# Kernel optimization log

Hardware: AMD Instinct MI355X
Metric: run time of the kernel (lower is better)

Reference implementation:

```python
import jax, jax.numpy as jnp
import numpy as np

B, LQ, LK, D = 2, 2048, 2048, 1024
H, DK, DV = 16, 64, 64
EPS = 1e-6


def setup_inputs() -> dict:
    key = jax.random.key(0)
    ks = jax.random.split(key, 12)
    s = 1.0 / np.sqrt(D)
    return {
        "PE_states": jax.random.normal(ks[0], (B, LK, D), jnp.float32),
        "global_state": jax.random.normal(ks[1], (B, LQ, D), jnp.float32),
        "PE_statements": jax.random.normal(ks[2], (B, LK, D), jnp.float32),
        "PE_operators": jax.random.normal(ks[3], (B, LK, D), jnp.float32),
        "PE_solution_scores": jax.random.uniform(ks[4], (B, LK), jnp.float32),
        "mask": jax.random.randint(ks[5], (B, LQ, LK), 0, 2, jnp.int32),
        "w_q": jax.random.normal(ks[6], (D, H * DK), jnp.float32) * s,
        "w_k": jax.random.normal(ks[7], (D, H * DK), jnp.float32) * s,
        "w_v": jax.random.normal(ks[8], (D, H * DV), jnp.float32) * s,
        "w_fc": jax.random.normal(ks[9], (H * DV, D), jnp.float32) * s,
        "ln_gamma": jnp.ones((D,), jnp.float32),
        "ln_beta": jnp.zeros((D,), jnp.float32),
    }


def _layer_norm(x, gamma, beta):
    mu = jnp.mean(x, axis=-1, keepdims=True)
    var = jnp.mean(jnp.square(x - mu), axis=-1, keepdims=True)
    return (x - mu) * jax.lax.rsqrt(var + EPS) * gamma + beta


def reference(PE_states, global_state, PE_statements, PE_operators,
              PE_solution_scores, mask, w_q, w_k, w_v, w_fc, ln_gamma, ln_beta):
    # att_type == 'ca_sc', query_mode == 'PE', dropout == 0
    residual = global_state  # [B, LQ, D]
    q = (global_state @ w_q).reshape(B, LQ, H, DK).transpose(0, 2, 1, 3)   # bhqd
    k = (PE_states @ w_k).reshape(B, LK, H, DK).transpose(0, 2, 1, 3)      # bhkd
    v_s = (PE_statements @ w_v).reshape(B, LK, H, DV).transpose(0, 2, 1, 3)
    v_o = (PE_operators @ w_v).reshape(B, LK, H, DV).transpose(0, 2, 1, 3)

    temp = jnp.asarray(DK, jnp.float32) ** 0.5
    attn = jnp.einsum('bhqd,bhkd->bhqk', q / temp, k)  # [B,H,LQ,LK]
    # PE_solution_scores: per-key bias broadcast over heads and queries
    attn = (attn + PE_solution_scores[:, None, None, :]) / 2.0
    attn = jnp.where(mask[:, None, :, :] == 0, jnp.float32(-1e9), attn)
    attn = jax.nn.softmax(attn, axis=-1)

    def head_out(v):
        o = jnp.einsum('bhqk,bhkd->bhqd', attn, v)
        o = o.transpose(0, 2, 1, 3).reshape(B, LQ, H * DV)
        o = o @ w_fc + residual
        return _layer_norm(o, ln_gamma, ln_beta)

    statement_pred = head_out(v_s)
    operator_pred = head_out(v_o)
    return statement_pred, operator_pred
```

## Files before the change

kernel.cpp:

```cpp
#include <hip/hip_runtime.h>


typedef unsigned short u16;
typedef unsigned int   u32;
typedef unsigned long long u64;

typedef __attribute__((ext_vector_type(8))) short frag_ab;
typedef __attribute__((ext_vector_type(4))) float frag_cd;
typedef __attribute__((ext_vector_type(16))) float f32x16;
typedef __attribute__((ext_vector_type(8))) unsigned short u16x8;
typedef __attribute__((ext_vector_type(4))) unsigned short u16x4;
typedef __attribute__((ext_vector_type(2))) unsigned int u32x2;
typedef __attribute__((ext_vector_type(4))) int int4v;

__device__ __forceinline__ u16 f2bf(float f) {
    u32 x = __builtin_bit_cast(u32, f);
    return (u16)((x + 0x7fffu + ((x >> 16) & 1u)) >> 16);
}

__device__ __forceinline__ u32 pkbf(float a, float b) {
    return __builtin_amdgcn_perm(__builtin_bit_cast(u32, b),
                                 __builtin_bit_cast(u32, a), 0x07060302u);
}

#define GLDS16(gsrc, ldst)                                                     \
    __builtin_amdgcn_global_load_lds(                                          \
        (const __attribute__((address_space(1))) void*)(gsrc),                 \
        (__attribute__((address_space(3))) void*)(ldst), 16, 0, 0)

#define MFMA32(a, b, c) __builtin_amdgcn_mfma_f32_32x32x16_bf16(a, b, c, 0, 0, 0)

__global__ __launch_bounds__(256) void prep_kernel(
    const float* __restrict__ in0, const float* __restrict__ in1,
    const float* __restrict__ in2, const float* __restrict__ in3,
    u16* __restrict__ Ab4,
    const float* __restrict__ w_q, const float* __restrict__ w_k,
    const float* __restrict__ w_v, const float* __restrict__ w_fc,
    u16* __restrict__ wqT, u16* __restrict__ wkT,
    u16* __restrict__ wvT, u16* __restrict__ wfcT,
    const int* __restrict__ mask, u64* __restrict__ bits)
{
    __shared__ u16 tile[32][33];
    const int bid = blockIdx.x;
    const int tid = threadIdx.x;
    if (bid < 8192) {
        int z = bid >> 11;
        const float* in = z == 0 ? in0 : z == 1 ? in1 : z == 2 ? in2 : in3;
        u16* o = Ab4 + (size_t)z * 4194304;
        size_t i = ((size_t)(bid & 2047) * 256 + tid) * 8;
        float4 f0 = *(const float4*)(in + i);
        float4 f1 = *(const float4*)(in + i + 4);
        u16x8 t;
        t[0] = f2bf(f0.x); t[1] = f2bf(f0.y); t[2] = f2bf(f0.z); t[3] = f2bf(f0.w);
        t[4] = f2bf(f1.x); t[5] = f2bf(f1.y); t[6] = f2bf(f1.z); t[7] = f2bf(f1.w);
        *(u16x8*)(o + i) = t;
    } else if (bid < 12288) {
        int t = bid - 8192;
        int z = t >> 10;
        const float* in = z == 0 ? w_q : z == 1 ? w_k : z == 2 ? w_v : w_fc;
        u16* out = z == 0 ? wqT : z == 1 ? wkT : z == 2 ? wvT : wfcT;
        int bx = (t & 31) * 32, by = ((t >> 5) & 31) * 32;
        int tx = tid & 31, ty = tid >> 5;
        for (int i = 0; i < 32; i += 8)
            tile[ty + i][tx] = f2bf(in[(size_t)(by + ty + i) * 1024 + bx + tx]);
        __syncthreads();
        for (int i = 0; i < 32; i += 8)
            out[(size_t)(bx + ty + i) * 1024 + by + tx] = tile[tx][ty + i];
    } else {
        int pb = bid - 12288;
        int wv = tid >> 6, ln = tid & 63;
        long long base = (long long)pb * 2048 + wv * 512;
        for (int j = 0; j < 8; j++) {
            int v = mask[base + j * 64 + ln];
            u64 bl = __ballot(v != 0);
            if (ln == 0) bits[(base >> 6) + j] = bl;
        }
    }
}

__device__ __forceinline__ void gemm256_core(
    const u16* __restrict__ A, const u16* __restrict__ BT,
    int bm, int bn, u16* ring, frag_cd acc[8][4])
{
    const int tid = threadIdx.x;
    const int wave = tid >> 6, lane = tid & 63;
    const int ln15 = lane & 15, quad = lane >> 4;
    const int wr = wave >> 2, wc = wave & 3;

    auto stage = [&](int t) {
        u16* slot = ring + (t & 3) * 16384;
        size_t col = (size_t)t * 32 + quad * 8;
        for (int s = 0; s < 4; s++) {
            int f = wave * 4 + s;
            if (f < 16)
                GLDS16(&A[(size_t)(bm + f * 16 + ln15) * 1024 + col], slot + f * 512);
            else
                GLDS16(&BT[(size_t)(bn + (f - 16) * 16 + ln15) * 1024 + col],
                       slot + 8192 + (f - 16) * 512);
        }
    };

    stage(0); stage(1); stage(2);

    for (int t = 0; t < 32; t++) {
        if (t < 30)       asm volatile("s_waitcnt vmcnt(8) lgkmcnt(0)" ::: "memory");
        else if (t == 30) asm volatile("s_waitcnt vmcnt(4) lgkmcnt(0)" ::: "memory");
        else              asm volatile("s_waitcnt vmcnt(0) lgkmcnt(0)" ::: "memory");
        __builtin_amdgcn_s_barrier();
        __builtin_amdgcn_sched_barrier(0);
        if (t < 29) stage(t + 3);
        const u16* slot = ring + (t & 3) * 16384;
        const u16* aBase = slot + wr * 8 * 512;
        const u16* bBase = slot + 8192 + wc * 4 * 512;
        frag_ab b[4];
#pragma unroll
        for (int j = 0; j < 4; j++)
            b[j] = *(const frag_ab*)(bBase + j * 512 + lane * 8);
#pragma unroll
        for (int m = 0; m < 8; m++) {
            frag_ab a = *(const frag_ab*)(aBase + m * 512 + lane * 8);
            __builtin_amdgcn_s_setprio(1);
#pragma unroll
            for (int j = 0; j < 4; j++)
                acc[m][j] = __builtin_amdgcn_mfma_f32_16x16x32_bf16(a, b[j], acc[m][j], 0, 0, 0);
            __builtin_amdgcn_s_setprio(0);
        }
    }
}

__global__ __launch_bounds__(512, 2) void proj_gemm_kernel(
    const u16* __restrict__ Ab4,
    const u16* __restrict__ wqT, const u16* __restrict__ wkT, const u16* __restrict__ wvT,
    u16* __restrict__ Qb, u16* __restrict__ Kb,
    u16* __restrict__ VsT_g, u16* __restrict__ VoT_g)
{
    __shared__ alignas(16) u16 ring[4 * 16384];
    const int bid = blockIdx.x;
    const int xcd = bid & 7;
    const int w = bid >> 3;
    const int z = xcd >> 1;
    const int bm = ((xcd & 1) * 8 + (w >> 2)) * 256;
    const int bn = (w & 3) * 256;
    const u16* A = Ab4 + (size_t)z * 4194304;
    const u16* BT = z == 0 ? wqT : z == 1 ? wkT : wvT;
    frag_cd acc[8][4] = {};
    gemm256_core(A, BT, bm, bn, ring, acc);

    const int lane = threadIdx.x & 63;
    const int wave = threadIdx.x >> 6;
    const int ln15 = lane & 15, quad = lane >> 4;
    const int wr = wave >> 2, wc = wave & 3;
    if (z < 2) {
        u16* C = z == 0 ? Qb : Kb;
        const float qsc = z == 0 ? 0.09016844f : 1.0f;
        for (int m = 0; m < 8; m++) for (int j = 0; j < 4; j++) {
            int row0 = bm + wr * 128 + m * 16 + quad * 4;
            int col = bn + wc * 64 + j * 16 + ln15;
            for (int r = 0; r < 4; r++)
                C[(size_t)(row0 + r) * 1024 + col] = f2bf(acc[m][j][r] * qsc);
        }
    } else {
        u16* C = z == 2 ? VsT_g : VoT_g;
        for (int m = 0; m < 8; m++) for (int j = 0; j < 4; j++) {
            int row0 = bm + wr * 128 + m * 16 + quad * 4;
            int col = bn + wc * 64 + j * 16 + ln15;
            u16x4 t;
            for (int r = 0; r < 4; r++) t[r] = f2bf(acc[m][j][r]);
            *(u16x4*)&C[(size_t)col * 4096 + row0] = t;
        }
    }
}

__global__ __launch_bounds__(512, 2) void fc_gemm_kernel(
    const u16* __restrict__ Osb, const u16* __restrict__ wfcT,
    const float* __restrict__ resid, float* __restrict__ preLN)
{
    __shared__ alignas(16) u16 ring[4 * 12288];
    const int bm = blockIdx.x * 256, bn = blockIdx.y * 128;
    const int tid = threadIdx.x;
    const int wave = tid >> 6, lane = tid & 63;
    const int ln15 = lane & 15, quad = lane >> 4;
    const int wr = wave >> 2, wc = wave & 3;
    const u16* A = Osb;
    frag_cd acc[8][2] = {};

    auto stage = [&](int t) {
        u16* slot = ring + (t & 3) * 12288;
        size_t col = (size_t)t * 32 + quad * 8;
        for (int s = 0; s < 3; s++) {
            int f = wave * 3 + s;
            if (f < 16)
                GLDS16(&A[(size_t)(bm + f * 16 + ln15) * 1024 + col], slot + f * 512);
            else
                GLDS16(&wfcT[(size_t)(bn + (f - 16) * 16 + ln15) * 1024 + col],
                       slot + 8192 + (f - 16) * 512);
        }
    };

    stage(0); stage(1); stage(2);

    for (int t = 0; t < 32; t++) {
        if (t < 30)       asm volatile("s_waitcnt vmcnt(6) lgkmcnt(0)" ::: "memory");
        else if (t == 30) asm volatile("s_waitcnt vmcnt(3) lgkmcnt(0)" ::: "memory");
        else              asm volatile("s_waitcnt vmcnt(0) lgkmcnt(0)" ::: "memory");
        __builtin_amdgcn_s_barrier();
        __builtin_amdgcn_sched_barrier(0);
        if (t < 29) stage(t + 3);
        const u16* slot = ring + (t & 3) * 12288;
        const u16* aBase = slot + wr * 8 * 512;
        const u16* bBase = slot + 8192 + wc * 2 * 512;
        frag_ab b[2];
#pragma unroll
        for (int j = 0; j < 2; j++)
            b[j] = *(const frag_ab*)(bBase + j * 512 + lane * 8);
#pragma unroll
        for (int m = 0; m < 8; m++) {
            frag_ab a = *(const frag_ab*)(aBase + m * 512 + lane * 8);
            __builtin_amdgcn_s_setprio(1);
#pragma unroll
            for (int j = 0; j < 2; j++)
                acc[m][j] = __builtin_amdgcn_mfma_f32_16x16x32_bf16(a, b[j], acc[m][j], 0, 0, 0);
            __builtin_amdgcn_s_setprio(0);
        }
    }

    for (int m = 0; m < 8; m++) for (int j = 0; j < 2; j++) {
        int row0 = bm + wr * 128 + m * 16 + quad * 4;
        int col = bn + wc * 32 + j * 16 + ln15;
        for (int r = 0; r < 4; r++) {
            int row = row0 + r;
            preLN[(size_t)row * 1024 + col] =
                acc[m][j][r] + resid[(size_t)(row & 4095) * 1024 + col];
        }
    }
}

__device__ __forceinline__ void flash_stage(
    const u16* __restrict__ Kp, const u16* __restrict__ VsT, const u16* __restrict__ VoT,
    int b, int h, int kt, int wave, int ln31, int hi, u16* buf)
{
    const int k0 = kt * 64;
    for (int s = 0; s < 6; s++) {
        int t = wave * 6 + s;
        const u16* g;
        if (t < 8) {
            int n = t >> 2, ks = t & 3;
            g = &Kp[(size_t)(b * 2048 + k0 + n * 32 + ln31) * 1024 + h * 64 + ks * 16 + hi * 8];
        } else if (t < 16) {
            int dt = (t >> 2) & 1, sk = t & 3;
            g = &VsT[(size_t)(h * 64 + dt * 32 + ln31) * 4096 + b * 2048 + k0 + sk * 16 + hi * 8];
        } else {
            int dt = (t >> 2) & 1, sk = t & 3;
            g = &VoT[(size_t)(h * 64 + dt * 32 + ln31) * 4096 + b * 2048 + k0 + sk * 16 + hi * 8];
        }
        GLDS16(g, buf + t * 512);
    }
}

__global__ __launch_bounds__(256, 2) void flash_kernel(
    const u16* __restrict__ Q, const u16* __restrict__ Kp,
    const u16* __restrict__ VsT_g, const u16* __restrict__ VoT_g,
    const float* __restrict__ scores, const u64* __restrict__ mbits,
    u16* __restrict__ Os, u16* __restrict__ Oo)
{
    __shared__ alignas(16) u16 KV[2][24 * 512];
    const int bid = blockIdx.x;
    const int xcd = bid & 7;
    const int qt = (bid >> 3) & 15;
    const int g = xcd + 8 * (bid >> 7);
    const int h = g & 15, b = g >> 4;
    const int tid = threadIdx.x;
    const int wave = tid >> 6, lane = tid & 63;
    const int ln31 = lane & 31, hi = lane >> 5;
    const int qbase = b * 2048 + qt * 128 + wave * 32;
    const int qrow = qbase + ln31;

    frag_ab aq0, aq1, aq2, aq3;
    {
        const u16* qp = &Q[(size_t)qrow * 1024 + h * 64 + hi * 8];
        aq0 = *(const frag_ab*)(qp);
        aq1 = *(const frag_ab*)(qp + 16);
        aq2 = *(const frag_ab*)(qp + 32);
        aq3 = *(const frag_ab*)(qp + 48);
    }
    frag_ab bbias = {};
    bbias[0] = (short)0x3F80; bbias[1] = (short)0x3F80;

    f32x16 os0 = {}, os1 = {}, oo0 = {}, oo1 = {};
    float l0 = 0.f, l1 = 0.f;
    const int shl4 = 4 - 4 * hi;

    auto softmax16 = [&](f32x16& s, u32 wa, float& lacc) {
#pragma unroll
        for (int r = 0; r < 16; r++) {
            const int bitc = (r & 3) + 8 * (r >> 2);
            u32 m = (u32)(((int)(wa << (27 - bitc))) >> 31);
            float e = __builtin_amdgcn_exp2f(s[r]);
            u32 pb = __builtin_bit_cast(u32, e) & m;
            float pf = __builtin_bit_cast(float, pb);
            lacc += pf;
            s[r] = pf;
        }
    };

    flash_stage(Kp, VsT_g, VoT_g, b, h, 0, wave, ln31, hi, KV[0]);

    for (int kt = 0; kt < 32; kt++) {
        const int p = kt & 1;
        float sc0f = scores[b * 2048 + kt * 64 + ln31];
        float sc1f = scores[b * 2048 + kt * 64 + 32 + ln31];
        u64 w = mbits[(size_t)qrow * 32 + kt];
        __syncthreads();
        if (kt < 31)
            flash_stage(Kp, VsT_g, VoT_g, b, h, kt + 1, wave, ln31, hi, KV[p ^ 1]);
        const u16* bufp = KV[p];

        frag_ab ab0 = {}, ab1 = {};
        if (!hi) {
            float t0 = sc0f * 0.72134752f;
            u16 c0 = f2bf(t0);
            ab0[0] = (short)c0;
            ab0[1] = (short)f2bf(t0 - __builtin_bit_cast(float, (u32)c0 << 16));
            float t1 = sc1f * 0.72134752f;
            u16 c1 = f2bf(t1);
            ab1[0] = (short)c1;
            ab1[1] = (short)f2bf(t1 - __builtin_bit_cast(float, (u32)c1 << 16));
        }

        f32x16 sacc0 = {}, sacc1 = {};
        sacc0 = MFMA32(ab0, bbias, sacc0);
        sacc1 = MFMA32(ab1, bbias, sacc1);
#pragma unroll
        for (int ks = 0; ks < 4; ks++) {
            frag_ab ak0 = *(const frag_ab*)(bufp + (0 * 4 + ks) * 512 + lane * 8);
            frag_ab ak1 = *(const frag_ab*)(bufp + (1 * 4 + ks) * 512 + lane * 8);
            frag_ab q = ks == 0 ? aq0 : ks == 1 ? aq1 : ks == 2 ? aq2 : aq3;
            sacc0 = MFMA32(ak0, q, sacc0);
            sacc1 = MFMA32(ak1, q, sacc1);
        }

        u32 wa0 = ((u32)w) << shl4;
        u32 wa1 = ((u32)(w >> 32)) << shl4;
        softmax16(sacc0, wa0, l0);
        softmax16(sacc1, wa1, l1);

#pragma unroll
        for (int sk = 0; sk < 4; sk++) {
            const f32x16& ps = (sk < 2) ? sacc0 : sacc1;
            const int e0 = (sk & 1) * 8;
            u32 a0 = pkbf(ps[e0 + 0], ps[e0 + 1]);
            u32 a1 = pkbf(ps[e0 + 2], ps[e0 + 3]);
            u32 b0 = pkbf(ps[e0 + 4], ps[e0 + 5]);
            u32 b1 = pkbf(ps[e0 + 6], ps[e0 + 7]);
            u32x2 r0 = __builtin_amdgcn_permlane32_swap(a0, b0, false, false);
            u32x2 r1 = __builtin_amdgcn_permlane32_swap(a1, b1, false, false);
            int4v iv;
            iv[0] = (int)r0[0]; iv[1] = (int)r1[0];
            iv[2] = (int)r0[1]; iv[3] = (int)r1[1];
            frag_ab ap = __builtin_bit_cast(frag_ab, iv);
            frag_ab bs0 = *(const frag_ab*)(bufp + (8 + sk) * 512 + lane * 8);
            frag_ab bs1 = *(const frag_ab*)(bufp + (12 + sk) * 512 + lane * 8);
            frag_ab bo0 = *(const frag_ab*)(bufp + (16 + sk) * 512 + lane * 8);
            frag_ab bo1 = *(const frag_ab*)(bufp + (20 + sk) * 512 + lane * 8);
            os0 = MFMA32(ap, bs0, os0);
            os1 = MFMA32(ap, bs1, os1);
            oo0 = MFMA32(ap, bo0, oo0);
            oo1 = MFMA32(ap, bo1, oo1);
        }
    }

    float l_run = l0 + l1;
    float l_tot = l_run + __shfl_xor(l_run, 32, 64);
#pragma unroll
    for (int r = 0; r < 16; r++) {
        const int qr = (r & 3) + 8 * (r >> 2) + 4 * hi;
        float lv = __shfl(l_tot, qr, 64);
        float inv = 1.0f / fmaxf(lv, 1e-30f);
        size_t row = (size_t)(qbase + qr) * 1024 + h * 64;
        Os[row + ln31]      = f2bf(os0[r] * inv);
        Os[row + 32 + ln31] = f2bf(os1[r] * inv);
        Oo[row + ln31]      = f2bf(oo0[r] * inv);
        Oo[row + 32 + ln31] = f2bf(oo1[r] * inv);
    }
}

__global__ __launch_bounds__(256) void ln_kernel(
    const float* __restrict__ X, const float* __restrict__ gamma, const float* __restrict__ beta,
    float* __restrict__ out)
{
    __shared__ float red[4];
    int row = blockIdx.x;
    int tid = threadIdx.x;
    const float* x = X + (size_t)row * 1024;
    float4 v = *(const float4*)(x + tid * 4);
    float s = v.x + v.y + v.z + v.w;
    for (int off = 1; off < 64; off <<= 1) s += __shfl_xor(s, off, 64);
    int wv = tid >> 6, ln = tid & 63;
    if (ln == 0) red[wv] = s;
    __syncthreads();
    float mean = (red[0] + red[1] + red[2] + red[3]) * (1.0f / 1024.0f);
    float dx = v.x - mean, dy = v.y - mean, dz = v.z - mean, dw = v.w - mean;
    float s2 = dx * dx + dy * dy + dz * dz + dw * dw;
    for (int off = 1; off < 64; off <<= 1) s2 += __shfl_xor(s2, off, 64);
    __syncthreads();
    if (ln == 0) red[wv] = s2;
    __syncthreads();
    float var = (red[0] + red[1] + red[2] + red[3]) * (1.0f / 1024.0f);
    float rstd = rsqrtf(var + 1e-6f);
    float4 gg = *(const float4*)(gamma + tid * 4);
    float4 bb = *(const float4*)(beta + tid * 4);
    float4 o;
    o.x = dx * rstd * gg.x + bb.x;
    o.y = dy * rstd * gg.y + bb.y;
    o.z = dz * rstd * gg.z + bb.z;
    o.w = dw * rstd * gg.w + bb.w;
    *(float4*)(out + (size_t)row * 1024 + tid * 4) = o;
}

extern "C" void kernel_launch(void* const* d_in, const int* in_sizes, int n_in,
                              void* d_out, int out_size, void* d_ws, size_t ws_size,
                              hipStream_t stream)
{
    const float* PE_states     = (const float*)d_in[0];
    const float* global_state  = (const float*)d_in[1];
    const float* PE_statements = (const float*)d_in[2];
    const float* PE_operators  = (const float*)d_in[3];
    const float* scores        = (const float*)d_in[4];
    const int*   mask          = (const int*)d_in[5];
    const float* w_q  = (const float*)d_in[6];
    const float* w_k  = (const float*)d_in[7];
    const float* w_v  = (const float*)d_in[8];
    const float* w_fc = (const float*)d_in[9];
    const float* gamma = (const float*)d_in[10];
    const float* beta  = (const float*)d_in[11];
    float* out = (float*)d_out;

    char* ws = (char*)d_ws;
    const size_t MB = 1u << 20;
    u16* Ab4   = (u16*)(ws + 0 * MB);
    u16* Osb   = (u16*)(ws + 0 * MB);
    u16* Oob   = (u16*)(ws + 8 * MB);
    u16* wqT   = (u16*)(ws + 32 * MB);
    u16* wkT   = (u16*)(ws + 34 * MB);
    u16* wvT   = (u16*)(ws + 36 * MB);
    u16* wfcT  = (u16*)(ws + 38 * MB);
    u64* mbits = (u64*)(ws + 40 * MB);
    u16* Qb    = (u16*)(ws + 41 * MB);
    u16* Kb    = (u16*)(ws + 49 * MB);
    u16* VsT_g = (u16*)(ws + 57 * MB);
    u16* VoT_g = (u16*)(ws + 65 * MB);
    float* preLN = (float*)(ws + 41 * MB);

    prep_kernel<<<16384, 256, 0, stream>>>(
        global_state, PE_states, PE_statements, PE_operators, Ab4,
        w_q, w_k, w_v, w_fc, wqT, wkT, wvT, wfcT, mask, mbits);

    proj_gemm_kernel<<<dim3(256), 512, 0, stream>>>(
        Ab4, wqT, wkT, wvT, Qb, Kb, VsT_g, VoT_g);

    flash_kernel<<<dim3(512), 256, 0, stream>>>(Qb, Kb, VsT_g, VoT_g, scores, mbits, Osb, Oob);

    fc_gemm_kernel<<<dim3(32, 8), 512, 0, stream>>>(Osb, wfcT, global_state, preLN);
    ln_kernel<<<8192, 256, 0, stream>>>(preLN, gamma, beta, out);
}
```

Measured before the change: 324.6 us.

## Software-pipeline PV MFMAs one tile behind QK with triple-buffered LDS

Defers the P·V matrix multiplies of each key tile to the next iteration, so they run after the next tile's QK^T and softmax and can overlap with its exp/mask ALU work. The packed probability fragments are carried across iterations in registers. LDS grows from two to three K/V buffers so the previous tile's V is still resident while the next tile is being staged. This costs extra LDS per block, which may limit occupancy at two blocks per CU, and more VGPRs for the carried fragments.

```diff
diff --git a/kernel.cpp b/kernel.cpp
--- a/kernel.cpp
+++ b/kernel.cpp
@@ -263,7 +263,7 @@
     const float* __restrict__ scores, const u64* __restrict__ mbits,
     u16* __restrict__ Os, u16* __restrict__ Oo)
 {
-    __shared__ alignas(16) u16 KV[2][24 * 512];
+    __shared__ alignas(16) u16 KV[3][24 * 512];
     const int bid = blockIdx.x;
     const int xcd = bid & 7;
     const int qt = (bid >> 3) & 15;
@@ -303,17 +303,18 @@
         }
     };
 
+    frag_ab pa0, pa1, pa2, pa3;
+
     flash_stage(Kp, VsT_g, VoT_g, b, h, 0, wave, ln31, hi, KV[0]);
 
     for (int kt = 0; kt < 32; kt++) {
-        const int p = kt & 1;
         float sc0f = scores[b * 2048 + kt * 64 + ln31];
         float sc1f = scores[b * 2048 + kt * 64 + 32 + ln31];
         u64 w = mbits[(size_t)qrow * 32 + kt];
         __syncthreads();
         if (kt < 31)
-            flash_stage(Kp, VsT_g, VoT_g, b, h, kt + 1, wave, ln31, hi, KV[p ^ 1]);
-        const u16* bufp = KV[p];
+            flash_stage(Kp, VsT_g, VoT_g, b, h, kt + 1, wave, ln31, hi, KV[(kt + 1) % 3]);
+        const u16* bufp = KV[kt % 3];
 
         frag_ab ab0 = {}, ab1 = {};
         if (!hi) {
@@ -343,6 +344,22 @@
         u32 wa1 = ((u32)(w >> 32)) << shl4;
         softmax16(sacc0, wa0, l0);
         softmax16(sacc1, wa1, l1);
+
+        if (kt > 0) {
+            const u16* vbuf = KV[(kt - 1) % 3];
+#pragma unroll
+            for (int sk = 0; sk < 4; sk++) {
+                frag_ab ap = sk == 0 ? pa0 : sk == 1 ? pa1 : sk == 2 ? pa2 : pa3;
+                frag_ab bs0 = *(const frag_ab*)(vbuf + (8 + sk) * 512 + lane * 8);
+                frag_ab bs1 = *(const frag_ab*)(vbuf + (12 + sk) * 512 + lane * 8);
+                frag_ab bo0 = *(const frag_ab*)(vbuf + (16 + sk) * 512 + lane * 8);
+                frag_ab bo1 = *(const frag_ab*)(vbuf + (20 + sk) * 512 + lane * 8);
+                os0 = MFMA32(ap, bs0, os0);
+                os1 = MFMA32(ap, bs1, os1);
+                oo0 = MFMA32(ap, bo0, oo0);
+                oo1 = MFMA32(ap, bo1, oo1);
+            }
+        }
 
 #pragma unroll
         for (int sk = 0; sk < 4; sk++) {
@@ -358,10 +375,20 @@
             iv[0] = (int)r0[0]; iv[1] = (int)r1[0];
             iv[2] = (int)r0[1]; iv[3] = (int)r1[1];
             frag_ab ap = __builtin_bit_cast(frag_ab, iv);
-            frag_ab bs0 = *(const frag_ab*)(bufp + (8 + sk) * 512 + lane * 8);
-            frag_ab bs1 = *(const frag_ab*)(bufp + (12 + sk) * 512 + lane * 8);
-            frag_ab bo0 = *(const frag_ab*)(bufp + (16 + sk) * 512 + lane * 8);
-            frag_ab bo1 = *(const frag_ab*)(bufp + (20 + sk) * 512 + lane * 8);
+            if (sk == 0) pa0 = ap; else if (sk == 1) pa1 = ap;
+            else if (sk == 2) pa2 = ap; else pa3 = ap;
+        }
+    }
+
+    {
+        const u16* vbuf = KV[31 % 3];
+#pragma unroll
+        for (int sk = 0; sk < 4; sk++) {
+            frag_ab ap = sk == 0 ? pa0 : sk == 1 ? pa1 : sk == 2 ? pa2 : pa3;
+            frag_ab bs0 = *(const frag_ab*)(vbuf + (8 + sk) * 512 + lane * 8);
+            frag_ab bs1 = *(const frag_ab*)(vbuf + (12 + sk) * 512 + lane * 8);
+            frag_ab bo0 = *(const frag_ab*)(vbuf + (16 + sk) * 512 + lane * 8);
+            frag_ab bo1 = *(const frag_ab*)(vbuf + (20 + sk) * 512 + lane * 8);
             os0 = MFMA32(ap, bs0, os0);
             os1 = MFMA32(ap, bs1, os1);
             oo0 = MFMA32(ap, bo0, oo0);
```

Measured after the change: 325.4 us. Within noise of the previous version (+0.3%).

## Fuse FC GEMM with residual add and LayerNorm into one kernel

Applied to the files above, without the earlier changes.

Replaces the separate FC GEMM and LayerNorm kernels with one kernel. Each block computes 32 full rows across all 1024 output columns, adds the residual, and reduces mean and variance in registers and shared memory before writing the normalized output. This removes the fp32 preLN round trip through global memory and one launch. In exchange each block reloads the whole wfc weight for only 32 rows, the ring shrinks to double buffering, and occupancy drops to one block per CU, so the GEMM itself may run less efficiently.

```diff
diff --git a/kernel.cpp b/kernel.cpp
--- a/kernel.cpp
+++ b/kernel.cpp
@@ -171,68 +171,133 @@
     }
 }
 
-__global__ __launch_bounds__(512, 2) void fc_gemm_kernel(
+__global__ __launch_bounds__(512, 1) void fcln_kernel(
     const u16* __restrict__ Osb, const u16* __restrict__ wfcT,
-    const float* __restrict__ resid, float* __restrict__ preLN)
-{
-    __shared__ alignas(16) u16 ring[4 * 12288];
-    const int bm = blockIdx.x * 256, bn = blockIdx.y * 128;
+    const float* __restrict__ resid,
+    const float* __restrict__ gamma, const float* __restrict__ beta,
+    float* __restrict__ out)
+{
+    __shared__ alignas(16) u16 ring[2 * 33792];
+    __shared__ float sums[8][32];
+    __shared__ float sums2[8][32];
+    const int brow = blockIdx.x * 32;
     const int tid = threadIdx.x;
     const int wave = tid >> 6, lane = tid & 63;
     const int ln15 = lane & 15, quad = lane >> 4;
-    const int wr = wave >> 2, wc = wave & 3;
     const u16* A = Osb;
-    frag_cd acc[8][2] = {};
+    frag_cd acc[2][8] = {};
 
     auto stage = [&](int t) {
-        u16* slot = ring + (t & 3) * 12288;
+        u16* slot = ring + (t & 1) * 33792;
         size_t col = (size_t)t * 32 + quad * 8;
-        for (int s = 0; s < 3; s++) {
-            int f = wave * 3 + s;
-            if (f < 16)
-                GLDS16(&A[(size_t)(bm + f * 16 + ln15) * 1024 + col], slot + f * 512);
-            else
-                GLDS16(&wfcT[(size_t)(bn + (f - 16) * 16 + ln15) * 1024 + col],
-                       slot + 8192 + (f - 16) * 512);
-        }
+        for (int s = 0; s < 8; s++) {
+            int g = wave * 8 + s;
+            GLDS16(&wfcT[(size_t)(g * 16 + ln15) * 1024 + col],
+                   slot + 1024 + g * 512);
+        }
+        if (wave < 2)
+            GLDS16(&A[(size_t)(brow + wave * 16 + ln15) * 1024 + col],
+                   slot + wave * 512);
     };
 
-    stage(0); stage(1); stage(2);
+    stage(0);
 
     for (int t = 0; t < 32; t++) {
-        if (t < 30)       asm volatile("s_waitcnt vmcnt(6) lgkmcnt(0)" ::: "memory");
-        else if (t == 30) asm volatile("s_waitcnt vmcnt(3) lgkmcnt(0)" ::: "memory");
-        else              asm volatile("s_waitcnt vmcnt(0) lgkmcnt(0)" ::: "memory");
-        __builtin_amdgcn_s_barrier();
-        __builtin_amdgcn_sched_barrier(0);
-        if (t < 29) stage(t + 3);
-        const u16* slot = ring + (t & 3) * 12288;
-        const u16* aBase = slot + wr * 8 * 512;
-        const u16* bBase = slot + 8192 + wc * 2 * 512;
-        frag_ab b[2];
-#pragma unroll
-        for (int j = 0; j < 2; j++)
-            b[j] = *(const frag_ab*)(bBase + j * 512 + lane * 8);
-#pragma unroll
-        for (int m = 0; m < 8; m++) {
-            frag_ab a = *(const frag_ab*)(aBase + m * 512 + lane * 8);
+        __syncthreads();
+        if (t < 31) stage(t + 1);
+        const u16* slot = ring + (t & 1) * 33792;
+        frag_ab a0 = *(const frag_ab*)(slot + 0 * 512 + lane * 8);
+        frag_ab a1 = *(const frag_ab*)(slot + 1 * 512 + lane * 8);
+#pragma unroll
+        for (int j = 0; j < 8; j++) {
+            frag_ab bj = *(const frag_ab*)(slot + 1024 + (wave * 8 + j) * 512 + lane * 8);
             __builtin_amdgcn_s_setprio(1);
-#pragma unroll
-            for (int j = 0; j < 2; j++)
-                acc[m][j] = __builtin_amdgcn_mfma_f32_16x16x32_bf16(a, b[j], acc[m][j], 0, 0, 0);
+            acc[0][j] = __builtin_amdgcn_mfma_f32_16x16x32_bf16(a0, bj, acc[0][j], 0, 0, 0);
+            acc[1][j] = __builtin_amdgcn_mfma_f32_16x16x32_bf16(a1, bj, acc[1][j], 0, 0, 0);
             __builtin_amdgcn_s_setprio(0);
         }
     }
 
-    for (int m = 0; m < 8; m++) for (int j = 0; j < 2; j++) {
-        int row0 = bm + wr * 128 + m * 16 + quad * 4;
-        int col = bn + wc * 32 + j * 16 + ln15;
+#pragma unroll
+    for (int m = 0; m < 2; m++)
+#pragma unroll
+        for (int j = 0; j < 8; j++) {
+            int col = wave * 128 + j * 16 + ln15;
+#pragma unroll
+            for (int r = 0; r < 4; r++) {
+                int rowg = brow + m * 16 + quad * 4 + r;
+                acc[m][j][r] += resid[(size_t)(rowg & 4095) * 1024 + col];
+            }
+        }
+
+    float ps[2][4];
+#pragma unroll
+    for (int m = 0; m < 2; m++)
+#pragma unroll
         for (int r = 0; r < 4; r++) {
-            int row = row0 + r;
-            preLN[(size_t)row * 1024 + col] =
-                acc[m][j][r] + resid[(size_t)(row & 4095) * 1024 + col];
-        }
-    }
+            float s = 0.f;
+#pragma unroll
+            for (int j = 0; j < 8; j++) s += acc[m][j][r];
+            for (int off = 1; off < 16; off <<= 1) s += __shfl_xor(s, off, 64);
+            ps[m][r] = s;
+        }
+    if (ln15 == 0)
+        for (int m = 0; m < 2; m++)
+            for (int r = 0; r < 4; r++)
+                sums[wave][m * 16 + quad * 4 + r] = ps[m][r];
+    __syncthreads();
+    float mean[2][4];
+#pragma unroll
+    for (int m = 0; m < 2; m++)
+#pragma unroll
+        for (int r = 0; r < 4; r++) {
+            int row = m * 16 + quad * 4 + r;
+            float s = 0.f;
+            for (int w = 0; w < 8; w++) s += sums[w][row];
+            mean[m][r] = s * (1.0f / 1024.0f);
+        }
+
+#pragma unroll
+    for (int m = 0; m < 2; m++)
+#pragma unroll
+        for (int r = 0; r < 4; r++) {
+            float s2 = 0.f;
+#pragma unroll
+            for (int j = 0; j < 8; j++) {
+                float d = acc[m][j][r] - mean[m][r];
+                s2 += d * d;
+            }
+            for (int off = 1; off < 16; off <<= 1) s2 += __shfl_xor(s2, off, 64);
+            ps[m][r] = s2;
+        }
+    if (ln15 == 0)
+        for (int m = 0; m < 2; m++)
+            for (int r = 0; r < 4; r++)
+                sums2[wave][m * 16 + quad * 4 + r] = ps[m][r];
+    __syncthreads();
+
+    float gg[8], bb[8];
+#pragma unroll
+    for (int j = 0; j < 8; j++) {
+        int col = wave * 128 + j * 16 + ln15;
+        gg[j] = gamma[col];
+        bb[j] = beta[col];
+    }
+#pragma unroll
+    for (int m = 0; m < 2; m++)
+#pragma unroll
+        for (int r = 0; r < 4; r++) {
+            int row = m * 16 + quad * 4 + r;
+            float s2 = 0.f;
+            for (int w = 0; w < 8; w++) s2 += sums2[w][row];
+            float rstd = rsqrtf(s2 * (1.0f / 1024.0f) + 1e-6f);
+            size_t base = (size_t)(brow + row) * 1024;
+#pragma unroll
+            for (int j = 0; j < 8; j++) {
+                int col = wave * 128 + j * 16 + ln15;
+                out[base + col] = (acc[m][j][r] - mean[m][r]) * rstd * gg[j] + bb[j];
+            }
+        }
 }
 
 __device__ __forceinline__ void flash_stage(
@@ -384,39 +449,6 @@
     }
 }
 
-__global__ __launch_bounds__(256) void ln_kernel(
-    const float* __restrict__ X, const float* __restrict__ gamma, const float* __restrict__ beta,
-    float* __restrict__ out)
-{
-    __shared__ float red[4];
-    int row = blockIdx.x;
-    int tid = threadIdx.x;
-    const float* x = X + (size_t)row * 1024;
-    float4 v = *(const float4*)(x + tid * 4);
-    float s = v.x + v.y + v.z + v.w;
-    for (int off = 1; off < 64; off <<= 1) s += __shfl_xor(s, off, 64);
-    int wv = tid >> 6, ln = tid & 63;
-    if (ln == 0) red[wv] = s;
-    __syncthreads();
-    float mean = (red[0] + red[1] + red[2] + red[3]) * (1.0f / 1024.0f);
-    float dx = v.x - mean, dy = v.y - mean, dz = v.z - mean, dw = v.w - mean;
-    float s2 = dx * dx + dy * dy + dz * dz + dw * dw;
-    for (int off = 1; off < 64; off <<= 1) s2 += __shfl_xor(s2, off, 64);
-    __syncthreads();
-    if (ln == 0) red[wv] = s2;
-    __syncthreads();
-    float var = (red[0] + red[1] + red[2] + red[3]) * (1.0f / 1024.0f);
-    float rstd = rsqrtf(var + 1e-6f);
-    float4 gg = *(const float4*)(gamma + tid * 4);
-    float4 bb = *(const float4*)(beta + tid * 4);
-    float4 o;
-    o.x = dx * rstd * gg.x + bb.x;
-    o.y = dy * rstd * gg.y + bb.y;
-    o.z = dz * rstd * gg.z + bb.z;
-    o.w = dw * rstd * gg.w + bb.w;
-    *(float4*)(out + (size_t)row * 1024 + tid * 4) = o;
-}
-
 extern "C" void kernel_launch(void* const* d_in, const int* in_sizes, int n_in,
                               void* d_out, int out_size, void* d_ws, size_t ws_size,
                               hipStream_t stream)
@@ -439,7 +471,6 @@
     const size_t MB = 1u << 20;
     u16* Ab4   = (u16*)(ws + 0 * MB);
     u16* Osb   = (u16*)(ws + 0 * MB);
-    u16* Oob   = (u16*)(ws + 8 * MB);
     u16* wqT   = (u16*)(ws + 32 * MB);
     u16* wkT   = (u16*)(ws + 34 * MB);
     u16* wvT   = (u16*)(ws + 36 * MB);
@@ -449,7 +480,7 @@
     u16* Kb    = (u16*)(ws + 49 * MB);
     u16* VsT_g = (u16*)(ws + 57 * MB);
     u16* VoT_g = (u16*)(ws + 65 * MB);
-    float* preLN = (float*)(ws + 41 * MB);
+    u16* Oob   = (u16*)(ws + 8 * MB);
 
     prep_kernel<<<16384, 256, 0, stream>>>(
         global_state, PE_states, PE_statements, PE_operators, Ab4,
@@ -460,6 +491,5 @@
 
     flash_kernel<<<dim3(512), 256, 0, stream>>>(Qb, Kb, VsT_g, VoT_g, scores, mbits, Osb, Oob);
 
-    fc_gemm_kernel<<<dim3(32, 8), 512, 0, stream>>>(Osb, wfcT, global_state, preLN);
-    ln_kernel<<<8192, 256, 0, stream>>>(preLN, gamma, beta, out);
-}
+    fcln_kernel<<<dim3(256), 512, 0, stream>>>(Osb, wfcT, global_state, gamma, beta, out);
+}
```

Measured after the change: 367.1 us. 1.13x slower.
